# Kernel optimization log

Hardware: AMD Instinct MI355X
Metric: run time of the kernel (lower is better)

The kernel has to match this reference:

```python
import jax, jax.numpy as jnp
import numpy as np

BLOCK_NUM = 1024

def setup_inputs() -> dict:
    key = jax.random.key(0)
    k1, k2 = jax.random.split(key)
    regional_means = jax.random.normal(k1, (32, BLOCK_NUM, 128), dtype=jnp.float32)
    adj = jax.random.uniform(k2, (32, BLOCK_NUM, BLOCK_NUM), dtype=jnp.float32)
    return {"regional_means": regional_means, "adj": adj}

def reference(regional_means, adj):
    # Original: adj_means[b,i,j,f] = adj[b,i,j] * regional_means[b,j,f],
    # diagonal (i==j) zeroed, then summed over j.
    # Algebraically: (adj with zeroed diagonal) @ regional_means.
    n = adj.shape[-1]
    mask = 1.0 - jnp.eye(n, dtype=adj.dtype)  # (n, n)
    adj_masked = adj * mask  # (b, n, n)
    # (b, n, n) @ (b, n, f) -> (b, n, f)
    return jnp.einsum('bij,bjf->bif', adj_masked, regional_means)
```

## Files before the change

kernel.cpp:

```cpp
#include <hip/hip_runtime.h>
#include <hip/hip_bf16.h>
#include <stdint.h>

typedef __attribute__((ext_vector_type(4))) float f32x4;
typedef __attribute__((ext_vector_type(2))) float f32x2;
typedef __attribute__((ext_vector_type(8))) short short8;
typedef __attribute__((ext_vector_type(4))) unsigned int u32x4;

__device__ __forceinline__ unsigned short f2bf(float x) {
  __hip_bfloat16 h = __float2bfloat16(x);
  union { __hip_bfloat16 b; unsigned short s; } u; u.b = h;
  return u.s;
}
__device__ __forceinline__ unsigned int pkbf(float lo, float hi) {
  return (unsigned int)f2bf(lo) | ((unsigned int)f2bf(hi) << 16);
}
__device__ __forceinline__ f32x4 ld4(const float* p) { return *(const f32x4*)p; }


#define MSK(v, k) (((k) == arow) ? 0.f : (v))

#define LOADA(kt, Aq) do {                                               \
    const float* p_ = aP + (kt) * 64;                                    \
    Aq[0] = ld4(p_); Aq[1] = ld4(p_ + 4);                                \
    Aq[2] = ld4(p_ + 32); Aq[3] = ld4(p_ + 36);                          \
  } while (0)

#define STAGE_LOAD(q1, h, S_) do {                                       \
    const float* p_ = bP0 + (q1) * 16384 + (h) * 4096;                   \
    _Pragma("unroll") for (int e_ = 0; e_ < 8; ++e_)                     \
      S_[e_] = *(const f32x2*)(p_ + e_ * 128);                           \
  } while (0)

#define STAGE_WRITE(nb, h, S_) do {                                      \
    u32x4 ua_, ub_;                                                      \
    ua_[0] = pkbf(S_[0].x, S_[1].x); ua_[1] = pkbf(S_[2].x, S_[3].x);    \
    ua_[2] = pkbf(S_[4].x, S_[5].x); ua_[3] = pkbf(S_[6].x, S_[7].x);    \
    ub_[0] = pkbf(S_[0].y, S_[1].y); ub_[1] = pkbf(S_[2].y, S_[3].y);    \
    ub_[2] = pkbf(S_[4].y, S_[5].y); ub_[3] = pkbf(S_[6].y, S_[7].y);    \
    char* p_ = wB + (nb) * 32768 + (h) * 1024;                           \
    *(u32x4*)p_ = ua_; *(u32x4*)(p_ + 16) = ub_;                         \
  } while (0)

#define COMPUTE(buf, kt, Aq) do {                                        \
    short8 af0_, af1_;                                                   \
    {                                                                    \
      union { u32x4 q; short8 s; } u0_, u1_;                             \
      if ((kt) == diag_kt) {                                             \
        const int jb_ = (kt) * 64 + kg;                                  \
        u0_.q[0] = pkbf(MSK(Aq[0][0], jb_ + 0),  MSK(Aq[0][1], jb_ + 1)); \
        u0_.q[1] = pkbf(MSK(Aq[0][2], jb_ + 2),  MSK(Aq[0][3], jb_ + 3)); \
        u0_.q[2] = pkbf(MSK(Aq[1][0], jb_ + 4),  MSK(Aq[1][1], jb_ + 5)); \
        u0_.q[3] = pkbf(MSK(Aq[1][2], jb_ + 6),  MSK(Aq[1][3], jb_ + 7)); \
        u1_.q[0] = pkbf(MSK(Aq[2][0], jb_ + 32), MSK(Aq[2][1], jb_ + 33)); \
        u1_.q[1] = pkbf(MSK(Aq[2][2], jb_ + 34), MSK(Aq[2][3], jb_ + 35)); \
        u1_.q[2] = pkbf(MSK(Aq[3][0], jb_ + 36), MSK(Aq[3][1], jb_ + 37)); \
        u1_.q[3] = pkbf(MSK(Aq[3][2], jb_ + 38), MSK(Aq[3][3], jb_ + 39)); \
      } else {                                                           \
        u0_.q[0] = pkbf(Aq[0][0], Aq[0][1]); u0_.q[1] = pkbf(Aq[0][2], Aq[0][3]); \
        u0_.q[2] = pkbf(Aq[1][0], Aq[1][1]); u0_.q[3] = pkbf(Aq[1][2], Aq[1][3]); \
        u1_.q[0] = pkbf(Aq[2][0], Aq[2][1]); u1_.q[1] = pkbf(Aq[2][2], Aq[2][3]); \
        u1_.q[2] = pkbf(Aq[3][0], Aq[3][1]); u1_.q[3] = pkbf(Aq[3][2], Aq[3][3]); \
      }                                                                  \
      af0_ = u0_.s; af1_ = u1_.s;                                        \
    }                                                                    \
    const char* base_ = rP + (buf) * 32768;                              \
    const int c_ = (kt) & 1;                                             \
    _Pragma("unroll")                                                    \
    for (int n_ = 0; n_ < 8; ++n_) {                                     \
      short8 bf0_ = *(const short8*)(base_ + (n_ * 4 + 2 * c_ + 0) * 1024); \
      acc[n_] = __builtin_amdgcn_mfma_f32_16x16x32_bf16(af0_, bf0_, acc[n_], 0, 0, 0); \
      short8 bf1_ = *(const short8*)(base_ + (n_ * 4 + 2 * c_ + 1) * 1024); \
      acc[n_] = __builtin_amdgcn_mfma_f32_16x16x32_bf16(af1_, bf1_, acc[n_], 0, 0, 0); \
    }                                                                    \
  } while (0)

__global__ __launch_bounds__(256, 2) void gcn_kernel(
    const float* __restrict__ means, const float* __restrict__ adj,
    float* __restrict__ out) {
  __shared__ char ldsB[65536];

  const int tid = (int)threadIdx.x;
  const int l = tid & 63;
  const int w = tid >> 6;
  const int bid = (int)blockIdx.x;
  const int batch = (bid & 7) * 4 + (bid >> 7);
  const int rtile = (bid >> 3) & 15;
  const int rbase = rtile * 64;

  const float* aB = adj + (size_t)batch * 1048576;
  const float* mB = means + (size_t)batch * 131072;
  float* oB = out + (size_t)batch * 131072;

  const int arow = rbase + w * 16 + (l & 15);
  const int kg = (l >> 4) * 8;
  const float* aP = aB + (size_t)arow * 1024 + kg;
  const int diag_kt = arow >> 6;

  const int n_t = tid >> 5;
  const int g_t = (tid >> 3) & 3;
  const int fc_t = (tid & 7) * 2;
  const float* bP0 = mB + (size_t)(g_t * 8) * 128 + n_t * 16 + fc_t;
  char* wB = ldsB + n_t * 4096 + g_t * 256 + fc_t * 16;
  const char* rP = ldsB + l * 16;

  f32x4 acc[8];
#pragma unroll
  for (int n = 0; n < 8; ++n) { f32x4 z = {0.f, 0.f, 0.f, 0.f}; acc[n] = z; }

  f32x4 Ar[2][4];

  {
    f32x2 S0[8], S1[8], S2[8], S3[8];
    STAGE_LOAD(0, 0, S0); STAGE_LOAD(0, 1, S1);
    STAGE_LOAD(0, 2, S2); STAGE_LOAD(0, 3, S3);
    LOADA(0, Ar[0]);
    STAGE_WRITE(0, 0, S0); STAGE_WRITE(0, 1, S1);
    STAGE_WRITE(0, 2, S2); STAGE_WRITE(0, 3, S3);
  }
  __syncthreads();

#pragma unroll
  for (int kt = 0; kt < 16; ++kt) {
    const int q = kt >> 1;
    const int c = kt & 1;
    const int buf = q & 1;
    const int nbuf = buf ^ 1;
    const int cur = kt & 1;
    const int nxt = cur ^ 1;

    if (kt < 15) LOADA(kt + 1, Ar[nxt]);

    f32x2 S0[8], S1[8];
    if (q < 7) {
      STAGE_LOAD(q + 1, 2 * c + 0, S0);
      STAGE_LOAD(q + 1, 2 * c + 1, S1);
    }

    COMPUTE(buf, kt, Ar[cur]);

    if (q < 7) {
      STAGE_WRITE(nbuf, 2 * c + 0, S0);
      STAGE_WRITE(nbuf, 2 * c + 1, S1);
    }
    if (c == 1) __syncthreads();
  }

  const int orow = rbase + w * 16 + (l >> 4) * 4;
  const int ocol = l & 15;
  float* op = oB + (size_t)orow * 128 + ocol;
#pragma unroll
  for (int n = 0; n < 8; ++n)
#pragma unroll
    for (int j = 0; j < 4; ++j)
      op[j * 128 + n * 16] = acc[n][j];
}

extern "C" void kernel_launch(void* const* d_in, const int* in_sizes, int n_in,
                              void* d_out, int out_size, void* d_ws, size_t ws_size,
                              hipStream_t stream) {
  const float* means = (const float*)d_in[0];
  const float* adj = (const float*)d_in[1];
  float* out = (float*)d_out;
  hipLaunchKernelGGL(gcn_kernel, dim3(512), dim3(256), 0, stream, means, adj, out);
}
```

Baseline: 216.4 us.

## Pre-convert means to bf16 MFMA layout and stream into LDS via global_load_lds

Adds a pre-pass kernel that converts regional_means to bf16 in the exact LDS fragment layout and writes it to workspace. The main kernel then fills LDS directly with global_load_lds, with no register staging or per-block conversion. Blocks grow to 512 threads covering 128 rows, which halves the grid to 256 blocks and halves redundant B traffic. The cost is an extra launch and an extra workspace round trip, plus a grid smaller than the CU count, which may leave some CUs idle.

```diff
diff --git a/kernel.cpp b/kernel.cpp
--- a/kernel.cpp
+++ b/kernel.cpp
@@ -3,7 +3,6 @@
 #include <stdint.h>
 
 typedef __attribute__((ext_vector_type(4))) float f32x4;
-typedef __attribute__((ext_vector_type(2))) float f32x2;
 typedef __attribute__((ext_vector_type(8))) short short8;
 typedef __attribute__((ext_vector_type(4))) unsigned int u32x4;
 
@@ -18,28 +17,34 @@
 __device__ __forceinline__ f32x4 ld4(const float* p) { return *(const f32x4*)p; }
 
 
+__global__ __launch_bounds__(256) void conv_means(
+    const float* __restrict__ means, u32x4* __restrict__ wsB) {
+  const int flat = (int)blockIdx.x * 256 + (int)threadIdx.x;
+  const int b = flat >> 14;
+  const int rem = flat & 16383;
+  const int q = rem >> 11;
+  const int idx16 = rem & 2047;
+  const int n = idx16 >> 8;
+  const int s = (idx16 >> 6) & 3;
+  const int ksub = (idx16 >> 4) & 3;
+  const int lc = idx16 & 15;
+  const int c = n * 16 + lc;
+  const int k0 = (q * 16 + s * 4 + ksub) * 8;
+  const float* src = means + ((size_t)b * 1024 + k0) * 128 + c;
+  u32x4 v;
+  v[0] = pkbf(src[0 * 128], src[1 * 128]);
+  v[1] = pkbf(src[2 * 128], src[3 * 128]);
+  v[2] = pkbf(src[4 * 128], src[5 * 128]);
+  v[3] = pkbf(src[6 * 128], src[7 * 128]);
+  wsB[flat] = v;
+}
+
 #define MSK(v, k) (((k) == arow) ? 0.f : (v))
 
 #define LOADA(kt, Aq) do {                                               \
     const float* p_ = aP + (kt) * 64;                                    \
     Aq[0] = ld4(p_); Aq[1] = ld4(p_ + 4);                                \
     Aq[2] = ld4(p_ + 32); Aq[3] = ld4(p_ + 36);                          \
-  } while (0)
-
-#define STAGE_LOAD(q1, h, S_) do {                                       \
-    const float* p_ = bP0 + (q1) * 16384 + (h) * 4096;                   \
-    _Pragma("unroll") for (int e_ = 0; e_ < 8; ++e_)                     \
-      S_[e_] = *(const f32x2*)(p_ + e_ * 128);                           \
-  } while (0)
-
-#define STAGE_WRITE(nb, h, S_) do {                                      \
-    u32x4 ua_, ub_;                                                      \
-    ua_[0] = pkbf(S_[0].x, S_[1].x); ua_[1] = pkbf(S_[2].x, S_[3].x);    \
-    ua_[2] = pkbf(S_[4].x, S_[5].x); ua_[3] = pkbf(S_[6].x, S_[7].x);    \
-    ub_[0] = pkbf(S_[0].y, S_[1].y); ub_[1] = pkbf(S_[2].y, S_[3].y);    \
-    ub_[2] = pkbf(S_[4].y, S_[5].y); ub_[3] = pkbf(S_[6].y, S_[7].y);    \
-    char* p_ = wB + (nb) * 32768 + (h) * 1024;                           \
-    *(u32x4*)p_ = ua_; *(u32x4*)(p_ + 16) = ub_;                         \
   } while (0)
 
 #define COMPUTE(buf, kt, Aq) do {                                        \
@@ -75,8 +80,17 @@
     }                                                                    \
   } while (0)
 
-__global__ __launch_bounds__(256, 2) void gcn_kernel(
-    const float* __restrict__ means, const float* __restrict__ adj,
+#define GLDSPHASE(nb, q1) do {                                           \
+    _Pragma("unroll")                                                    \
+    for (int call_ = 0; call_ < 4; ++call_) {                            \
+      const u32x4* g_ = wsB + wsBase + (q1) * 2048 + call_ * 512 + w * 64 + l; \
+      char* d_ = ldsB + (nb) * 32768 + call_ * 8192 + w * 1024;          \
+      __builtin_amdgcn_global_load_lds((const uint32_t*)g_, (uint32_t*)d_, 16, 0, 0); \
+    }                                                                    \
+  } while (0)
+
+__global__ __launch_bounds__(512) void gcn_kernel(
+    const float* __restrict__ adj, const u32x4* __restrict__ wsB,
     float* __restrict__ out) {
   __shared__ char ldsB[65536];
 
@@ -84,24 +98,19 @@
   const int l = tid & 63;
   const int w = tid >> 6;
   const int bid = (int)blockIdx.x;
-  const int batch = (bid & 7) * 4 + (bid >> 7);
-  const int rtile = (bid >> 3) & 15;
-  const int rbase = rtile * 64;
+  const int batch = (bid & 7) * 4 + (bid >> 6);
+  const int rtile = (bid >> 3) & 7;
+  const int rbase = rtile * 128;
 
   const float* aB = adj + (size_t)batch * 1048576;
-  const float* mB = means + (size_t)batch * 131072;
   float* oB = out + (size_t)batch * 131072;
+  const size_t wsBase = (size_t)batch * 16384;
 
   const int arow = rbase + w * 16 + (l & 15);
   const int kg = (l >> 4) * 8;
   const float* aP = aB + (size_t)arow * 1024 + kg;
   const int diag_kt = arow >> 6;
 
-  const int n_t = tid >> 5;
-  const int g_t = (tid >> 3) & 3;
-  const int fc_t = (tid & 7) * 2;
-  const float* bP0 = mB + (size_t)(g_t * 8) * 128 + n_t * 16 + fc_t;
-  char* wB = ldsB + n_t * 4096 + g_t * 256 + fc_t * 16;
   const char* rP = ldsB + l * 16;
 
   f32x4 acc[8];
@@ -110,14 +119,8 @@
 
   f32x4 Ar[2][4];
 
-  {
-    f32x2 S0[8], S1[8], S2[8], S3[8];
-    STAGE_LOAD(0, 0, S0); STAGE_LOAD(0, 1, S1);
-    STAGE_LOAD(0, 2, S2); STAGE_LOAD(0, 3, S3);
-    LOADA(0, Ar[0]);
-    STAGE_WRITE(0, 0, S0); STAGE_WRITE(0, 1, S1);
-    STAGE_WRITE(0, 2, S2); STAGE_WRITE(0, 3, S3);
-  }
+  GLDSPHASE(0, 0);
+  LOADA(0, Ar[0]);
   __syncthreads();
 
 #pragma unroll
@@ -129,20 +132,9 @@
     const int cur = kt & 1;
     const int nxt = cur ^ 1;
 
+    if (c == 0 && q < 7) GLDSPHASE(nbuf, q + 1);
     if (kt < 15) LOADA(kt + 1, Ar[nxt]);
-
-    f32x2 S0[8], S1[8];
-    if (q < 7) {
-      STAGE_LOAD(q + 1, 2 * c + 0, S0);
-      STAGE_LOAD(q + 1, 2 * c + 1, S1);
-    }
-
     COMPUTE(buf, kt, Ar[cur]);
-
-    if (q < 7) {
-      STAGE_WRITE(nbuf, 2 * c + 0, S0);
-      STAGE_WRITE(nbuf, 2 * c + 1, S1);
-    }
     if (c == 1) __syncthreads();
   }
 
@@ -162,5 +154,9 @@
   const float* means = (const float*)d_in[0];
   const float* adj = (const float*)d_in[1];
   float* out = (float*)d_out;
-  hipLaunchKernelGGL(gcn_kernel, dim3(512), dim3(256), 0, stream, means, adj, out);
+  u32x4* wsB = (u32x4*)d_ws;
+
+  hipLaunchKernelGGL(conv_means, dim3(2048), dim3(256), 0, stream, means, wsB);
+  hipLaunchKernelGGL(gcn_kernel, dim3(256), dim3(512), 0, stream,
+                     adj, (const u32x4*)wsB, out);
 }
```

Measured after the change: 219.7 us. About the same (+1.5%).
